# Optimization experiments

Hardware: AMD Instinct MI355X
Metric: run time of the kernel (lower is better)

## Reference

```python
import jax, jax.numpy as jnp
import numpy as np

N = 200000   # nodes
E = 6400000  # edges (avg degree 32)
T = 6        # member feature dim
M = 10       # fingerprint dim
L = 4        # R + 1 layers
GIN = 14     # group_level_input
GLO = 10     # group_level_output


def setup_inputs() -> dict:
    key = jax.random.key(0)
    ks = jax.random.split(key, 10)
    return {
        "x_member": jax.random.normal(ks[0], (N, T), dtype=jnp.float32),
        "x_group": jax.random.normal(ks[1], (1, GIN), dtype=jnp.float32),
        "src": jax.random.randint(ks[2], (E,), 0, N, dtype=jnp.int32),
        "dst": jax.random.randint(ks[3], (E,), 0, N, dtype=jnp.int32),
        "H": jax.random.normal(ks[4], (L, T, M), dtype=jnp.float32),
        "W": jax.random.normal(ks[5], (L,), dtype=jnp.float32),
        "gW": jax.random.normal(ks[6], (GLO, GIN), dtype=jnp.float32) * 0.1,
        "gb": jax.random.normal(ks[7], (GLO,), dtype=jnp.float32),
        "mW": jax.random.normal(ks[8], (3, M + GLO), dtype=jnp.float32) * 0.1,
        "mb": jax.random.normal(ks[9], (3,), dtype=jnp.float32),
    }


def reference(x_member, x_group, src, dst, H, W, gW, gb, mW, mb):
    n = x_member.shape[0]
    # message passing: neighbor feature sum per destination node  [N, T]
    neigh = jax.ops.segment_sum(x_member[src], dst, num_segments=n)
    v1 = x_member + neigh  # r[a] + sum of neighbor r's; r is layer-invariant
    # all R+1 layers at once: [L, N, M]
    v2 = jax.nn.sigmoid(jnp.einsum("nt,ltm->lnm", v1, H))
    fl = jax.nn.softmax(v2 * W[:, None, None], axis=-1)
    # f starts at zeros and accumulates softmax over every node and layer -> [1, M]
    f = jnp.sum(fl, axis=(0, 1))[None, :]
    # group-level perceptron
    g = jax.nn.sigmoid(x_group @ gW.T + gb)  # [1, GLO]
    merged = jnp.concatenate([f, g], axis=1)  # [1, M+GLO]
    return jax.nn.softmax(merged @ mW.T + mb, axis=-1)  # [1, 3]
```

## Files before the change

### kernel.cpp

```cpp
#include <hip/hip_runtime.h>
#include <hip/hip_fp16.h>
#include <math.h>

#define TDIM 6
#define MDIM 10
#define LDIM 4
#define GIND 14
#define GLOD 10

#define BINSHIFT 8
#define BINSZ 256
#define MAXBINS 1024

#define SC2_BLOCKS 1024
#define SC2_THREADS 512
#define SC2_CHQ 800
#define SC2_CHUNKS 2
#define SC2_TQ 2
#define OVF_ENT 16384
#define META2 2048

#define SC_BLOCK 512
#define SC_EPT 32
#define SC_EPB (SC_BLOCK * SC_EPT)
#define AC_BLOCK 512
#define AC_CAP 8704
#define AC_EPT 17

#define SRT_HALF 4352
#define AH_EPT 9
#define PB_NODE (BINSZ * TDIM)

__global__ void zero32_k(unsigned* __restrict__ p, int n) {
    int i = blockIdx.x * blockDim.x + threadIdx.x;
    if (i < n) p[i] = 0u;
}

__device__ __forceinline__ void add_row4(uint4 r, float& s0, float& s1, float& s2,
                                         float& s3, float& s4, float& s5) {
    float2 a0 = __half22float2(*(__half2*)&r.x);
    float2 a1 = __half22float2(*(__half2*)&r.y);
    float2 a2 = __half22float2(*(__half2*)&r.z);
    s0 += a0.x; s1 += a0.y; s2 += a1.x; s3 += a1.y; s4 += a2.x; s5 += a2.y;
}


__global__ __launch_bounds__(SC2_THREADS) void scat2_k(
        const float* __restrict__ xm, int N, uint4* __restrict__ xh,
        const int* __restrict__ src, const int* __restrict__ dst, int E, int NQ, int QPB,
        unsigned* __restrict__ gcount, unsigned* __restrict__ ebuf, int C, int nbins,
        uint2* __restrict__ ovf, unsigned* __restrict__ ocur) {
    __shared__ unsigned lcount[MAXBINS];
    __shared__ unsigned lbase[MAXBINS];
    __shared__ unsigned lcur[MAXBINS];
    __shared__ unsigned cstart[MAXBINS];
    __shared__ unsigned wsum[8];
    __shared__ unsigned spk[SC2_CHQ * 4];
    __shared__ unsigned short sbin[SC2_CHQ * 4];
    int tid = threadIdx.x;
    for (int i = tid; i < MAXBINS; i += SC2_THREADS) { lcount[i] = 0u; lcur[i] = 0u; }

    int gid = blockIdx.x * SC2_THREADS + tid;
    int gstride = gridDim.x * SC2_THREADS;
    for (int n = gid; n < N; n += gstride) {
        const float2* r = (const float2*)(xm + (size_t)n * TDIM);
        float2 a = r[0], b = r[1], c = r[2];
        __half2 h0 = __floats2half2_rn(a.x, a.y);
        __half2 h1 = __floats2half2_rn(b.x, b.y);
        __half2 h2 = __floats2half2_rn(c.x, c.y);
        uint4 o;
        o.x = *(unsigned*)&h0; o.y = *(unsigned*)&h1; o.z = *(unsigned*)&h2; o.w = 0u;
        xh[n] = o;
    }
    if (blockIdx.x == 0) {
        for (int e = NQ * 4 + tid; e < E; e += SC2_THREADS) {
            unsigned oc = atomicAdd(ocur, 1u);
            if (oc < OVF_ENT) ovf[oc] = make_uint2((unsigned)src[e], (unsigned)dst[e]);
        }
    }
    __syncthreads();

    int qb = blockIdx.x * QPB;
    int qend = qb + QPB; if (qend > NQ) qend = NQ;
    const int4* s4p = (const int4*)src;
    const int4* d4p = (const int4*)dst;

    for (int q = qb + tid; q < qend; q += SC2_THREADS) {
        int4 dv = d4p[q];
        atomicAdd(&lcount[((unsigned)dv.x) >> BINSHIFT], 1u);
        atomicAdd(&lcount[((unsigned)dv.y) >> BINSHIFT], 1u);
        atomicAdd(&lcount[((unsigned)dv.z) >> BINSHIFT], 1u);
        atomicAdd(&lcount[((unsigned)dv.w) >> BINSHIFT], 1u);
    }
    __syncthreads();
    for (int i = tid; i < nbins; i += SC2_THREADS) {
        unsigned c = lcount[i];
        if (c) lbase[i] = atomicAdd(&gcount[i], c);
    }
    __syncthreads();

    for (int ch = 0; ch < SC2_CHUNKS; ch++) {
        int cb = qb + ch * SC2_CHQ;
        if (cb >= qend) break;
        int ce = cb + SC2_CHQ; if (ce > qend) ce = qend;
        for (int i = tid; i < MAXBINS; i += SC2_THREADS) lcount[i] = 0u;
        __syncthreads();

        unsigned pk[SC2_TQ * 4];
        unsigned wr[SC2_TQ * 4];
#pragma unroll
        for (int i = 0; i < SC2_TQ; i++) {
            int q = cb + tid + i * SC2_THREADS;
            if (q < ce) {
                int4 sv = s4p[q];
                int4 dv = d4p[q];
                {
                    unsigned du = (unsigned)dv.x, b = du >> BINSHIFT;
                    pk[i*4+0] = ((du & (BINSZ-1)) << 18) | (unsigned)sv.x;
                    wr[i*4+0] = (b << 18) | atomicAdd(&lcount[b], 1u);
                }
                {
                    unsigned du = (unsigned)dv.y, b = du >> BINSHIFT;
                    pk[i*4+1] = ((du & (BINSZ-1)) << 18) | (unsigned)sv.y;
                    wr[i*4+1] = (b << 18) | atomicAdd(&lcount[b], 1u);
                }
                {
                    unsigned du = (unsigned)dv.z, b = du >> BINSHIFT;
                    pk[i*4+2] = ((du & (BINSZ-1)) << 18) | (unsigned)sv.z;
                    wr[i*4+2] = (b << 18) | atomicAdd(&lcount[b], 1u);
                }
                {
                    unsigned du = (unsigned)dv.w, b = du >> BINSHIFT;
                    pk[i*4+3] = ((du & (BINSZ-1)) << 18) | (unsigned)sv.w;
                    wr[i*4+3] = (b << 18) | atomicAdd(&lcount[b], 1u);
                }
            } else {
                pk[i*4+0] = 0xFFFFFFFFu; pk[i*4+1] = 0xFFFFFFFFu;
                pk[i*4+2] = 0xFFFFFFFFu; pk[i*4+3] = 0xFFFFFFFFu;
            }
        }
        __syncthreads();

        unsigned a0 = lcount[2*tid], a1 = lcount[2*tid+1];
        {
            unsigned s = a0 + a1;
            int lane = tid & 63;
#pragma unroll
            for (int off = 1; off < 64; off <<= 1) {
                unsigned t = (unsigned)__shfl_up((int)s, off, 64);
                if (lane >= off) s += t;
            }
            if (lane == 63) wsum[tid >> 6] = s;
            __syncthreads();
            unsigned add = 0; int w = tid >> 6;
#pragma unroll
            for (int ww = 0; ww < 7; ww++) if (ww < w) add += wsum[ww];
            unsigned excl = s + add - (a0 + a1);
            cstart[2*tid] = excl;
            cstart[2*tid+1] = excl + a0;
        }
        __syncthreads();

#pragma unroll
        for (int k = 0; k < SC2_TQ * 4; k++) {
            unsigned p = pk[k];
            if (p != 0xFFFFFFFFu) {
                unsigned b = wr[k] >> 18;
                unsigned r = wr[k] & 0x3FFFFu;
                unsigned li = cstart[b] + r;
                spk[li] = p;
                sbin[li] = (unsigned short)b;
            }
        }
        __syncthreads();

        unsigned T = cstart[MAXBINS-1] + lcount[MAXBINS-1];
        for (unsigned j = tid; j < T; j += SC2_THREADS) {
            unsigned p = spk[j];
            unsigned b = (unsigned)sbin[j];
            unsigned pos = lbase[b] + lcur[b] + (j - cstart[b]);
            if (pos < (unsigned)C) {
                ebuf[b * (unsigned)C + pos] = p;
            } else {
                unsigned oc = atomicAdd(ocur, 1u);
                if (oc < OVF_ENT) {
                    ovf[oc] = make_uint2(p & 0x3FFFFu,
                                         (b << BINSHIFT) | (p >> 18));
                }
            }
        }
        lcur[2*tid]   += a0;
        lcur[2*tid+1] += a1;
        __syncthreads();
    }
}

__global__ __launch_bounds__(512) void accum_a_k(
        const uint4* __restrict__ xh,
        const unsigned* __restrict__ ebuf, const unsigned* __restrict__ gcount, int C,
        const unsigned* __restrict__ ocur, const uint2* __restrict__ ovf,
        float* __restrict__ pbuf, int nbins) {
    __shared__ unsigned srt[SRT_HALF];
    __shared__ unsigned cnt[BINSZ];
    __shared__ unsigned cstart[BINSZ];
    __shared__ unsigned wsum[4];
    __shared__ unsigned ovl[256];
    __shared__ unsigned ovn;
    float (*part)[BINSZ][TDIM] = (float(*)[BINSZ][TDIM])srt;
    int tid = threadIdx.x;
    int bh = blockIdx.x;
    int bin = bh >> 1;
    unsigned half = (unsigned)(bh & 1);
    if (tid < BINSZ) cnt[tid] = 0u;
    if (tid == 0) ovn = 0u;
    __syncthreads();

    unsigned gc = gcount[bin];
    unsigned m = gc < (unsigned)C ? gc : (unsigned)C;
    unsigned lo = half ? (m >> 1) : 0u;
    unsigned hi = half ? m : (m >> 1);
    unsigned e0 = (unsigned)bin * (unsigned)C;

    unsigned ed_[AH_EPT];
    unsigned rk_[AH_EPT];
#pragma unroll
    for (int k = 0; k < AH_EPT; k++) {
        ed_[k] = 0xFFFFFFFFu;
        unsigned i = lo + (unsigned)tid + (unsigned)k * 512u;
        if (i < hi) {
            unsigned v = __builtin_nontemporal_load(ebuf + e0 + i);
            ed_[k] = v;
            rk_[k] = atomicAdd(&cnt[v >> 18], 1u);
        }
    }
    if (half == 0u) {
        unsigned novf = *ocur;
        if (novf > OVF_ENT) novf = OVF_ENT;
        for (unsigned i = tid; i < novf; i += 512u) {
            uint2 e = ovf[i];
            if ((e.y >> BINSHIFT) == (unsigned)bin) {
                unsigned u = atomicAdd(&ovn, 1u);
                if (u < 256u) ovl[u] = ((e.y & (BINSZ-1)) << 18) | e.x;
            }
        }
    }
    __syncthreads();

    {
        unsigned v = (tid < BINSZ) ? cnt[tid] : 0u;
        int lane = tid & 63;
#pragma unroll
        for (int off = 1; off < 64; off <<= 1) {
            unsigned t = (unsigned)__shfl_up((int)v, off, 64);
            if (lane >= off) v += t;
        }
        if (tid < BINSZ && lane == 63) wsum[tid >> 6] = v;
        __syncthreads();
        if (tid < BINSZ) {
            unsigned add = 0;
            int w = tid >> 6;
#pragma unroll
            for (int ww = 0; ww < 3; ww++) if (ww < w) add += wsum[ww];
            cstart[tid] = v + add - cnt[tid];
        }
        __syncthreads();
    }

#pragma unroll
    for (int k = 0; k < AH_EPT; k++) {
        unsigned v = ed_[k];
        if (v != 0xFFFFFFFFu) srt[cstart[v >> 18] + rk_[k]] = v & 0x3FFFFu;
    }
    __syncthreads();

    int node = tid & (BINSZ - 1);
    int role = tid >> 8;
    float s0 = 0.f, s1 = 0.f, s2 = 0.f, s3 = 0.f, s4 = 0.f, s5 = 0.f;
    {
        unsigned c = cnt[node];
        unsigned b0 = cstart[node];
        unsigned h2 = c >> 1;
        unsigned j  = role ? h2 : 0u;
        unsigned je = role ? c : h2;
        for (; j + 8 <= je; j += 8) {
            unsigned i0 = srt[b0 + j],     i1 = srt[b0 + j + 1];
            unsigned i2 = srt[b0 + j + 2], i3 = srt[b0 + j + 3];
            unsigned i4 = srt[b0 + j + 4], i5 = srt[b0 + j + 5];
            unsigned i6 = srt[b0 + j + 6], i7 = srt[b0 + j + 7];
            uint4 r0 = xh[i0], r1 = xh[i1], r2 = xh[i2], r3 = xh[i3];
            uint4 r4 = xh[i4], r5 = xh[i5], r6 = xh[i6], r7 = xh[i7];
            add_row4(r0, s0, s1, s2, s3, s4, s5);
            add_row4(r1, s0, s1, s2, s3, s4, s5);
            add_row4(r2, s0, s1, s2, s3, s4, s5);
            add_row4(r3, s0, s1, s2, s3, s4, s5);
            add_row4(r4, s0, s1, s2, s3, s4, s5);
            add_row4(r5, s0, s1, s2, s3, s4, s5);
            add_row4(r6, s0, s1, s2, s3, s4, s5);
            add_row4(r7, s0, s1, s2, s3, s4, s5);
        }
        for (; j + 2 <= je; j += 2) {
            unsigned ia = srt[b0 + j], ib = srt[b0 + j + 1];
            uint4 ra = xh[ia], rb = xh[ib];
            add_row4(ra, s0, s1, s2, s3, s4, s5);
            add_row4(rb, s0, s1, s2, s3, s4, s5);
        }
        if (j < je) {
            uint4 ra = xh[srt[b0 + j]];
            add_row4(ra, s0, s1, s2, s3, s4, s5);
        }
        if (role == 0) {
            unsigned no = ovn < 256u ? ovn : 256u;
            for (unsigned q = 0; q < no; q++) {
                unsigned o = ovl[q];
                if ((int)(o >> 18) == node) {
                    uint4 rr = xh[o & 0x3FFFFu];
                    add_row4(rr, s0, s1, s2, s3, s4, s5);
                }
            }
        }
    }
    __syncthreads();
    part[role][node][0] = s0; part[role][node][1] = s1; part[role][node][2] = s2;
    part[role][node][3] = s3; part[role][node][4] = s4; part[role][node][5] = s5;
    __syncthreads();

    float* pb = pbuf + (size_t)bh * PB_NODE;
    for (int j = tid; j < PB_NODE; j += 512) {
        int nd = j / TDIM, d = j - nd * TDIM;
        pb[j] = part[0][nd][d] + part[1][nd][d];
    }
}

__global__ __launch_bounds__(256) void accum_b_k(
        const float* __restrict__ xm, const float* __restrict__ pbuf,
        const float* __restrict__ H, const float* __restrict__ W,
        float* __restrict__ facc, int N) {
    __shared__ float sH[LDIM * TDIM * MDIM];
    __shared__ float sW[LDIM];
    __shared__ float sred[4][MDIM];
    int tid = threadIdx.x;
    for (int i = tid; i < LDIM * TDIM * MDIM; i += 256) sH[i] = H[i];
    if (tid < LDIM) sW[tid] = W[tid];
    __syncthreads();

    int n = blockIdx.x * 256 + tid;
    float fs[MDIM];
#pragma unroll
    for (int mm = 0; mm < MDIM; mm++) fs[mm] = 0.f;

    if (n < N) {
        int bin = n >> BINSHIFT;
        int node = n & (BINSZ - 1);
        const float* p0 = pbuf + (size_t)(bin * 2 + 0) * PB_NODE + node * TDIM;
        const float* p1 = pbuf + (size_t)(bin * 2 + 1) * PB_NODE + node * TDIM;
        const float2* xr = (const float2*)(xm + (size_t)n * TDIM);
        float2 x0 = xr[0], x1 = xr[1], x2 = xr[2];
        float v[TDIM];
        v[0] = x0.x + p0[0] + p1[0];
        v[1] = x0.y + p0[1] + p1[1];
        v[2] = x1.x + p0[2] + p1[2];
        v[3] = x1.y + p0[3] + p1[3];
        v[4] = x2.x + p0[4] + p1[4];
        v[5] = x2.y + p0[5] + p1[5];

#pragma unroll
        for (int l = 0; l < LDIM; l++) {
            float z[MDIM];
#pragma unroll
            for (int mm = 0; mm < MDIM; mm++) {
                float a2 = 0.f;
#pragma unroll
                for (int t = 0; t < TDIM; t++) a2 += v[t] * sH[(l * TDIM + t) * MDIM + mm];
                z[mm] = a2;
            }
            float wl = sW[l];
            float mx = -1e30f;
#pragma unroll
            for (int mm = 0; mm < MDIM; mm++) {
                float sg = wl / (1.f + __expf(-z[mm]));
                z[mm] = sg;
                mx = fmaxf(mx, sg);
            }
            float se = 0.f;
#pragma unroll
            for (int mm = 0; mm < MDIM; mm++) {
                float e = __expf(z[mm] - mx);
                z[mm] = e;
                se += e;
            }
            float inv = 1.f / se;
#pragma unroll
            for (int mm = 0; mm < MDIM; mm++) fs[mm] += z[mm] * inv;
        }
    }

#pragma unroll
    for (int mm = 0; mm < MDIM; mm++) {
        float v = fs[mm];
#pragma unroll
        for (int off = 32; off > 0; off >>= 1) v += __shfl_down(v, off, 64);
        fs[mm] = v;
    }
    int wave = tid >> 6, lane = tid & 63;
    if (lane == 0) {
#pragma unroll
        for (int mm = 0; mm < MDIM; mm++) sred[wave][mm] = fs[mm];
    }
    __syncthreads();
    if (tid < MDIM) {
        float s = 0.f;
#pragma unroll
        for (int w = 0; w < 4; w++) s += sred[w][tid];
        atomicAdd(facc + tid, s);
    }
}

__global__ __launch_bounds__(AC_BLOCK) void accum2_k(
        const float* __restrict__ xm, const uint4* __restrict__ xh,
        const unsigned* __restrict__ ebuf, const unsigned* __restrict__ gcount, int C,
        const unsigned* __restrict__ ocur, const uint2* __restrict__ ovf,
        const float* __restrict__ H, const float* __restrict__ W,
        float* __restrict__ facc, int N) {
    __shared__ unsigned srt[AC_CAP];
    __shared__ unsigned cnt[BINSZ];
    __shared__ unsigned cstart[BINSZ];
    __shared__ unsigned wsum[8];
    __shared__ unsigned ovl[256];
    __shared__ unsigned ovn;
    __shared__ float sH[LDIM * TDIM * MDIM];
    __shared__ float sW[LDIM];
    __shared__ float sred[AC_BLOCK / 64][MDIM];
    float (*part)[BINSZ][TDIM] = (float(*)[BINSZ][TDIM])srt;
    int tid = threadIdx.x;
    int bin = blockIdx.x;
    for (int i = tid; i < LDIM * TDIM * MDIM; i += AC_BLOCK) sH[i] = H[i];
    if (tid < LDIM) sW[tid] = W[tid];
    if (tid < BINSZ) cnt[tid] = 0u;
    if (tid == 0) ovn = 0u;
    __syncthreads();

    unsigned gc = gcount[bin];
    unsigned m = gc < (unsigned)C ? gc : (unsigned)C;
    unsigned e0 = (unsigned)bin * (unsigned)C;
    int nbase = bin << BINSHIFT;

    unsigned ed_[AC_EPT];
    unsigned rk_[AC_EPT];
#pragma unroll
    for (int k = 0; k < AC_EPT; k++) {
        unsigned i = (unsigned)tid + (unsigned)k * AC_BLOCK;
        if (i < m) {
            unsigned v = __builtin_nontemporal_load(ebuf + e0 + i);
            ed_[k] = v;
            rk_[k] = atomicAdd(&cnt[v >> 18], 1u);
        }
    }
    {
        unsigned novf = *ocur;
        if (novf > OVF_ENT) novf = OVF_ENT;
        for (unsigned i = tid; i < novf; i += AC_BLOCK) {
            uint2 e = ovf[i];
            if ((e.y >> BINSHIFT) == (unsigned)bin) {
                unsigned u = atomicAdd(&ovn, 1u);
                if (u < 256u) ovl[u] = ((e.y & (BINSZ-1)) << 18) | e.x;
            }
        }
    }
    __syncthreads();

    {
        unsigned v = (tid < BINSZ) ? cnt[tid] : 0u;
        int lane = tid & 63;
#pragma unroll
        for (int off = 1; off < 64; off <<= 1) {
            unsigned t = (unsigned)__shfl_up((int)v, off, 64);
            if (lane >= off) v += t;
        }
        if (tid < BINSZ && lane == 63) wsum[tid >> 6] = v;
        __syncthreads();
        if (tid < BINSZ) {
            unsigned add = 0;
            int w = tid >> 6;
#pragma unroll
            for (int ww = 0; ww < 3; ww++) if (ww < w) add += wsum[ww];
            cstart[tid] = v + add - cnt[tid];
        }
        __syncthreads();
    }

#pragma unroll
    for (int k = 0; k < AC_EPT; k++) {
        unsigned i = (unsigned)tid + (unsigned)k * AC_BLOCK;
        if (i < m) {
            unsigned v = ed_[k];
            srt[cstart[v >> 18] + rk_[k]] = v & 0x3FFFFu;
        }
    }
    __syncthreads();

    int node = tid & (BINSZ - 1);
    int role = tid >> 8;
    int n = nbase + node;
    float s0 = 0.f, s1 = 0.f, s2 = 0.f, s3 = 0.f, s4 = 0.f, s5 = 0.f;
    if (n < N) {
        unsigned c = cnt[node];
        unsigned b0 = cstart[node];
        unsigned h = c >> 1;
        unsigned j  = role ? h : 0u;
        unsigned je = role ? c : h;
        for (; j + 8 <= je; j += 8) {
            unsigned i0 = srt[b0 + j],     i1 = srt[b0 + j + 1];
            unsigned i2 = srt[b0 + j + 2], i3 = srt[b0 + j + 3];
            unsigned i4 = srt[b0 + j + 4], i5 = srt[b0 + j + 5];
            unsigned i6 = srt[b0 + j + 6], i7 = srt[b0 + j + 7];
            uint4 r0 = xh[i0], r1 = xh[i1], r2 = xh[i2], r3 = xh[i3];
            uint4 r4 = xh[i4], r5 = xh[i5], r6 = xh[i6], r7 = xh[i7];
            add_row4(r0, s0, s1, s2, s3, s4, s5);
            add_row4(r1, s0, s1, s2, s3, s4, s5);
            add_row4(r2, s0, s1, s2, s3, s4, s5);
            add_row4(r3, s0, s1, s2, s3, s4, s5);
            add_row4(r4, s0, s1, s2, s3, s4, s5);
            add_row4(r5, s0, s1, s2, s3, s4, s5);
            add_row4(r6, s0, s1, s2, s3, s4, s5);
            add_row4(r7, s0, s1, s2, s3, s4, s5);
        }
        for (; j + 2 <= je; j += 2) {
            unsigned ia = srt[b0 + j], ib = srt[b0 + j + 1];
            uint4 ra = xh[ia], rb = xh[ib];
            add_row4(ra, s0, s1, s2, s3, s4, s5);
            add_row4(rb, s0, s1, s2, s3, s4, s5);
        }
        if (j < je) {
            uint4 ra = xh[srt[b0 + j]];
            add_row4(ra, s0, s1, s2, s3, s4, s5);
        }
        if (role == 0) {
            unsigned no = ovn < 256u ? ovn : 256u;
            for (unsigned q = 0; q < no; q++) {
                unsigned o = ovl[q];
                if ((int)(o >> 18) == node) {
                    uint4 rr = xh[o & 0x3FFFFu];
                    add_row4(rr, s0, s1, s2, s3, s4, s5);
                }
            }
        }
    }
    __syncthreads();
    part[role][node][0] = s0; part[role][node][1] = s1; part[role][node][2] = s2;
    part[role][node][3] = s3; part[role][node][4] = s4; part[role][node][5] = s5;
    __syncthreads();

    float fs[MDIM];
#pragma unroll
    for (int mm = 0; mm < MDIM; mm++) fs[mm] = 0.f;

    if (n < N) {
        float v[TDIM];
        const float2* xr = (const float2*)(xm + (size_t)n * TDIM);
        float2 x0 = xr[0], x1 = xr[1], x2 = xr[2];
        v[0] = x0.x + part[0][node][0] + part[1][node][0];
        v[1] = x0.y + part[0][node][1] + part[1][node][1];
        v[2] = x1.x + part[0][node][2] + part[1][node][2];
        v[3] = x1.y + part[0][node][3] + part[1][node][3];
        v[4] = x2.x + part[0][node][4] + part[1][node][4];
        v[5] = x2.y + part[0][node][5] + part[1][node][5];

        int lb = role << 1;
#pragma unroll
        for (int li = 0; li < 2; li++) {
            int l = lb + li;
            float z[MDIM];
#pragma unroll
            for (int mm = 0; mm < MDIM; mm++) {
                float a2 = 0.f;
#pragma unroll
                for (int t = 0; t < TDIM; t++) a2 += v[t] * sH[(l * TDIM + t) * MDIM + mm];
                z[mm] = a2;
            }
            float wl = sW[l];
            float mx = -1e30f;
#pragma unroll
            for (int mm = 0; mm < MDIM; mm++) {
                float sg = wl / (1.f + __expf(-z[mm]));
                z[mm] = sg;
                mx = fmaxf(mx, sg);
            }
            float se = 0.f;
#pragma unroll
            for (int mm = 0; mm < MDIM; mm++) {
                float e = __expf(z[mm] - mx);
                z[mm] = e;
                se += e;
            }
            float inv = 1.f / se;
#pragma unroll
            for (int mm = 0; mm < MDIM; mm++) fs[mm] += z[mm] * inv;
        }
    }

#pragma unroll
    for (int mm = 0; mm < MDIM; mm++) {
        float v = fs[mm];
#pragma unroll
        for (int off = 32; off > 0; off >>= 1) v += __shfl_down(v, off, 64);
        fs[mm] = v;
    }
    int wave = tid >> 6, lane = tid & 63;
    if (lane == 0) {
#pragma unroll
        for (int mm = 0; mm < MDIM; mm++) sred[wave][mm] = fs[mm];
    }
    __syncthreads();
    if (tid < MDIM) {
        float s = 0.f;
#pragma unroll
        for (int w = 0; w < AC_BLOCK / 64; w++) s += sred[w][tid];
        atomicAdd(facc + tid, s);
    }
}


__global__ __launch_bounds__(256) void prep_k(const float* __restrict__ xm, int N,
                                              uint4* __restrict__ xh,
                                              const int* __restrict__ dst, int E,
                                              unsigned* __restrict__ hist, int nbins) {
    __shared__ unsigned lh[MAXBINS];
    for (int i = threadIdx.x; i < MAXBINS; i += blockDim.x) lh[i] = 0u;
    __syncthreads();
    int gid = blockIdx.x * blockDim.x + threadIdx.x;
    int gstride = gridDim.x * blockDim.x;
    for (int n = gid; n < N; n += gstride) {
        const float2* r = (const float2*)(xm + (size_t)n * TDIM);
        float2 a = r[0], b = r[1], c = r[2];
        __half2 h0 = __floats2half2_rn(a.x, a.y);
        __half2 h1 = __floats2half2_rn(b.x, b.y);
        __half2 h2 = __floats2half2_rn(c.x, c.y);
        uint4 o;
        o.x = *(unsigned*)&h0; o.y = *(unsigned*)&h1; o.z = *(unsigned*)&h2; o.w = 0u;
        xh[n] = o;
    }
    int e4 = E >> 2;
    const int4* d4p = (const int4*)dst;
    for (int i = gid; i < e4; i += gstride) {
        int4 d = d4p[i];
        atomicAdd(&lh[((unsigned)d.x) >> BINSHIFT], 1u);
        atomicAdd(&lh[((unsigned)d.y) >> BINSHIFT], 1u);
        atomicAdd(&lh[((unsigned)d.z) >> BINSHIFT], 1u);
        atomicAdd(&lh[((unsigned)d.w) >> BINSHIFT], 1u);
    }
    for (int e = (e4 << 2) + gid; e < E; e += gstride)
        atomicAdd(&lh[((unsigned)dst[e]) >> BINSHIFT], 1u);
    __syncthreads();
    for (int i = threadIdx.x; i < nbins; i += blockDim.x)
        if (lh[i]) atomicAdd(&hist[i], lh[i]);
}

__global__ __launch_bounds__(MAXBINS) void scan_k(const unsigned* __restrict__ hist,
                                                  unsigned* __restrict__ offsets,
                                                  unsigned* __restrict__ gfill, int nbins) {
    __shared__ unsigned buf[2][MAXBINS];
    int t = threadIdx.x;
    buf[0][t] = (t < nbins) ? hist[t] : 0u;
    __syncthreads();
    int cur = 0;
    for (int off = 1; off < MAXBINS; off <<= 1) {
        unsigned v = buf[cur][t];
        if (t >= off) v += buf[cur][t - off];
        buf[cur ^ 1][t] = v;
        __syncthreads();
        cur ^= 1;
    }
    if (t < nbins) {
        unsigned ex = t ? buf[cur][t - 1] : 0u;
        offsets[t] = ex;
        gfill[t] = ex;
    }
    if (t == 0) offsets[nbins] = buf[cur][nbins - 1];
}

__global__ __launch_bounds__(SC_BLOCK) void scatter_k(const int* __restrict__ src,
                                                      const int* __restrict__ dst, int E,
                                                      unsigned* __restrict__ gfill,
                                                      unsigned* __restrict__ ebuf, int nbins) {
    __shared__ unsigned lcount[MAXBINS];
    __shared__ unsigned lbase[MAXBINS];
    for (int i = threadIdx.x; i < MAXBINS; i += SC_BLOCK) lcount[i] = 0u;
    __syncthreads();
    int base = blockIdx.x * SC_EPB + threadIdx.x * SC_EPT;
    int s[SC_EPT], d[SC_EPT];
    unsigned rk[SC_EPT];
#pragma unroll
    for (int q = 0; q < SC_EPT / 4; q++) {
        int e = base + q * 4;
        if (e + 3 < E) {
            int4 s4 = *(const int4*)(src + e);
            int4 d4 = *(const int4*)(dst + e);
            s[q*4+0] = s4.x; s[q*4+1] = s4.y; s[q*4+2] = s4.z; s[q*4+3] = s4.w;
            d[q*4+0] = d4.x; d[q*4+1] = d4.y; d[q*4+2] = d4.z; d[q*4+3] = d4.w;
        } else {
#pragma unroll
            for (int k = 0; k < 4; k++) {
                int ee = e + k;
                s[q*4+k] = (ee < E) ? src[ee] : -1;
                d[q*4+k] = (ee < E) ? dst[ee] : 0;
            }
        }
    }
#pragma unroll
    for (int k = 0; k < SC_EPT; k++)
        if (s[k] >= 0) rk[k] = atomicAdd(&lcount[((unsigned)d[k]) >> BINSHIFT], 1u);
    __syncthreads();
    for (int i = threadIdx.x; i < nbins; i += SC_BLOCK) {
        unsigned c = lcount[i];
        if (c) lbase[i] = atomicAdd(&gfill[i], c);
    }
    __syncthreads();
#pragma unroll
    for (int k = 0; k < SC_EPT; k++) {
        if (s[k] >= 0) {
            unsigned du = (unsigned)d[k];
            unsigned b = du >> BINSHIFT;
            unsigned pack = ((du & (BINSZ - 1)) << 18) | (unsigned)s[k];
            ebuf[lbase[b] + rk[k]] = pack;
        }
    }
}

__global__ __launch_bounds__(AC_BLOCK) void accum_node_k(
        const float* __restrict__ xm, const uint4* __restrict__ xh,
        const unsigned* __restrict__ ebuf, const unsigned* __restrict__ offsets,
        const float* __restrict__ H, const float* __restrict__ W,
        float* __restrict__ facc, int N) {
    __shared__ unsigned srt[AC_CAP];
    __shared__ unsigned cnt[BINSZ];
    __shared__ unsigned tmp[BINSZ];
    __shared__ unsigned cstart[BINSZ];
    __shared__ float sH[LDIM * TDIM * MDIM];
    __shared__ float sW[LDIM];
    __shared__ float sred[AC_BLOCK / 64][MDIM];
    int tid = threadIdx.x;
    int bin = blockIdx.x;
    for (int i = tid; i < LDIM * TDIM * MDIM; i += AC_BLOCK) sH[i] = H[i];
    if (tid < LDIM) sW[tid] = W[tid];
    if (tid < BINSZ) cnt[tid] = 0u;
    __syncthreads();

    unsigned e0 = offsets[bin], e1 = offsets[bin + 1];
    unsigned total = e1 - e0;
    unsigned m = total < AC_CAP ? total : AC_CAP;
    int nbase = bin << BINSHIFT;

    unsigned ed_[AC_EPT];
    unsigned rk_[AC_EPT];
#pragma unroll
    for (int k = 0; k < AC_EPT; k++) {
        unsigned idx = e0 + (unsigned)tid + (unsigned)k * AC_BLOCK;
        if (idx < e0 + m) {
            unsigned v = ebuf[idx];
            ed_[k] = v;
            rk_[k] = atomicAdd(&cnt[v >> 18], 1u);
        }
    }
    __syncthreads();

    if (tid < BINSZ) tmp[tid] = cnt[tid];
    __syncthreads();
    for (int off = 1; off < BINSZ; off <<= 1) {
        unsigned v = 0;
        if (tid < BINSZ) { v = tmp[tid]; if (tid >= off) v += tmp[tid - off]; }
        __syncthreads();
        if (tid < BINSZ) tmp[tid] = v;
        __syncthreads();
    }
    if (tid < BINSZ) cstart[tid] = tmp[tid] - cnt[tid];
    __syncthreads();

#pragma unroll
    for (int k = 0; k < AC_EPT; k++) {
        unsigned idx = e0 + (unsigned)tid + (unsigned)k * AC_BLOCK;
        if (idx < e0 + m) {
            unsigned v = ed_[k];
            srt[cstart[v >> 18] + rk_[k]] = v & 0x3FFFFu;
        }
    }
    __syncthreads();

    float fs[MDIM];
#pragma unroll
    for (int mm = 0; mm < MDIM; mm++) fs[mm] = 0.f;

    int n = nbase + tid;
    if (tid < BINSZ && n < N) {
        float s0 = 0.f, s1 = 0.f, s2 = 0.f, s3 = 0.f, s4 = 0.f, s5 = 0.f;
        unsigned c = cnt[tid];
        unsigned b0 = cstart[tid];
        unsigned j = 0;
        for (; j + 2 <= c; j += 2) {
            unsigned sa = srt[b0 + j], sb = srt[b0 + j + 1];
            uint4 ra = xh[sa];
            uint4 rb = xh[sb];
            add_row4(ra, s0, s1, s2, s3, s4, s5);
            add_row4(rb, s0, s1, s2, s3, s4, s5);
        }
        if (j < c) {
            uint4 ra = xh[srt[b0 + j]];
            add_row4(ra, s0, s1, s2, s3, s4, s5);
        }
        for (unsigned idx = e0 + m; idx < e1; idx++) {
            unsigned v = ebuf[idx];
            if ((int)(v >> 18) == tid) {
                uint4 ra = xh[v & 0x3FFFFu];
                add_row4(ra, s0, s1, s2, s3, s4, s5);
            }
        }

        float v[TDIM];
        const float2* xr = (const float2*)(xm + (size_t)n * TDIM);
        float2 x0 = xr[0], x1 = xr[1], x2 = xr[2];
        v[0] = x0.x + s0; v[1] = x0.y + s1;
        v[2] = x1.x + s2; v[3] = x1.y + s3;
        v[4] = x2.x + s4; v[5] = x2.y + s5;

#pragma unroll
        for (int l = 0; l < LDIM; l++) {
            float z[MDIM];
#pragma unroll
            for (int mm = 0; mm < MDIM; mm++) {
                float a2 = 0.f;
#pragma unroll
                for (int t = 0; t < TDIM; t++) a2 += v[t] * sH[(l * TDIM + t) * MDIM + mm];
                z[mm] = a2;
            }
            float wl = sW[l];
            float mx = -1e30f;
#pragma unroll
            for (int mm = 0; mm < MDIM; mm++) {
                float sg = wl / (1.f + __expf(-z[mm]));
                z[mm] = sg;
                mx = fmaxf(mx, sg);
            }
            float se = 0.f;
#pragma unroll
            for (int mm = 0; mm < MDIM; mm++) {
                float e = __expf(z[mm] - mx);
                z[mm] = e;
                se += e;
            }
            float inv = 1.f / se;
#pragma unroll
            for (int mm = 0; mm < MDIM; mm++) fs[mm] += z[mm] * inv;
        }
    }

#pragma unroll
    for (int mm = 0; mm < MDIM; mm++) {
        float v = fs[mm];
#pragma unroll
        for (int off = 32; off > 0; off >>= 1) v += __shfl_down(v, off, 64);
        fs[mm] = v;
    }
    int wave = tid >> 6, lane = tid & 63;
    if (lane == 0) {
#pragma unroll
        for (int mm = 0; mm < MDIM; mm++) sred[wave][mm] = fs[mm];
    }
    __syncthreads();
    if (tid < MDIM) {
        float s = 0.f;
#pragma unroll
        for (int w = 0; w < AC_BLOCK / 64; w++) s += sred[w][tid];
        atomicAdd(facc + tid, s);
    }
}

__global__ void finalize_k(const float* __restrict__ facc,
                           const float* __restrict__ xg,
                           const float* __restrict__ gW,
                           const float* __restrict__ gb,
                           const float* __restrict__ mW,
                           const float* __restrict__ mb,
                           float* __restrict__ out) {
    if (threadIdx.x == 0 && blockIdx.x == 0) {
        float merged[MDIM + GLOD];
#pragma unroll
        for (int m = 0; m < MDIM; m++) merged[m] = facc[m];
        for (int j = 0; j < GLOD; j++) {
            float a = gb[j];
            for (int i = 0; i < GIND; i++) a += xg[i] * gW[j * GIND + i];
            merged[MDIM + j] = 1.f / (1.f + __expf(-a));
        }
        float lg[3];
        float mx = -1e30f;
        for (int k = 0; k < 3; k++) {
            float a = mb[k];
            for (int j = 0; j < MDIM + GLOD; j++) a += merged[j] * mW[k * (MDIM + GLOD) + j];
            lg[k] = a;
            mx = fmaxf(mx, a);
        }
        float se = 0.f;
        for (int k = 0; k < 3; k++) { lg[k] = __expf(lg[k] - mx); se += lg[k]; }
        float inv = 1.f / se;
        for (int k = 0; k < 3; k++) out[k] = lg[k] * inv;
    }
}

__global__ void fb_zero_k(float* __restrict__ ws, int n) {
    int i = blockIdx.x * blockDim.x + threadIdx.x;
    if (i < n) ws[i] = 0.f;
}

__global__ void fb_edge_scatter_k(const float* __restrict__ xm,
                                  const int* __restrict__ src,
                                  const int* __restrict__ dst,
                                  float* __restrict__ neigh, int E) {
    int e = blockIdx.x * blockDim.x + threadIdx.x;
    if (e >= E) return;
    int s = src[e], d = dst[e];
    const float2* r = (const float2*)(xm + (size_t)s * TDIM);
    float2 a = r[0], b = r[1], c = r[2];
    float* o = neigh + (size_t)d * TDIM;
    atomicAdd(o + 0, a.x); atomicAdd(o + 1, a.y);
    atomicAdd(o + 2, b.x); atomicAdd(o + 3, b.y);
    atomicAdd(o + 4, c.x); atomicAdd(o + 5, c.y);
}

__global__ __launch_bounds__(256) void fb_node_k(
        const float* __restrict__ xm, const float* __restrict__ neigh,
        const float* __restrict__ H, const float* __restrict__ W,
        float* __restrict__ facc, int N) {
    __shared__ float sH[LDIM * TDIM * MDIM];
    __shared__ float sW[LDIM];
    __shared__ float sred[4][MDIM];
    int tid = threadIdx.x;
    for (int i = tid; i < LDIM * TDIM * MDIM; i += blockDim.x) sH[i] = H[i];
    if (tid < LDIM) sW[tid] = W[tid];
    __syncthreads();
    float fs[MDIM];
#pragma unroll
    for (int m = 0; m < MDIM; m++) fs[m] = 0.f;
    for (int n = blockIdx.x * blockDim.x + tid; n < N; n += gridDim.x * blockDim.x) {
        float v[TDIM];
        const float2* xr = (const float2*)(xm + (size_t)n * TDIM);
        const float2* nr = (const float2*)(neigh + (size_t)n * TDIM);
#pragma unroll
        for (int t2 = 0; t2 < 3; t2++) {
            float2 a = xr[t2], b = nr[t2];
            v[2 * t2 + 0] = a.x + b.x;
            v[2 * t2 + 1] = a.y + b.y;
        }
#pragma unroll
        for (int l = 0; l < LDIM; l++) {
            float z[MDIM];
#pragma unroll
            for (int m = 0; m < MDIM; m++) {
                float a2 = 0.f;
#pragma unroll
                for (int t = 0; t < TDIM; t++) a2 += v[t] * sH[(l * TDIM + t) * MDIM + m];
                z[m] = a2;
            }
            float wl = sW[l], mx = -1e30f;
#pragma unroll
            for (int m = 0; m < MDIM; m++) { float sg = wl / (1.f + __expf(-z[m])); z[m] = sg; mx = fmaxf(mx, sg); }
            float se = 0.f;
#pragma unroll
            for (int m = 0; m < MDIM; m++) { float e = __expf(z[m] - mx); z[m] = e; se += e; }
            float inv = 1.f / se;
#pragma unroll
            for (int m = 0; m < MDIM; m++) fs[m] += z[m] * inv;
        }
    }
#pragma unroll
    for (int m = 0; m < MDIM; m++) {
        float v = fs[m];
#pragma unroll
        for (int off = 32; off > 0; off >>= 1) v += __shfl_down(v, off, 64);
        fs[m] = v;
    }
    int wave = tid >> 6, lane = tid & 63;
    if (lane == 0) {
#pragma unroll
        for (int m = 0; m < MDIM; m++) sred[wave][m] = fs[m];
    }
    __syncthreads();
    if (tid < MDIM) {
        float s = sred[0][tid] + sred[1][tid] + sred[2][tid] + sred[3][tid];
        atomicAdd(facc + tid, s);
    }
}

extern "C" void kernel_launch(void* const* d_in, const int* in_sizes, int n_in,
                              void* d_out, int out_size, void* d_ws, size_t ws_size,
                              hipStream_t stream) {
    const float* xm  = (const float*)d_in[0];
    const float* xg  = (const float*)d_in[1];
    const int*   src = (const int*)d_in[2];
    const int*   dst = (const int*)d_in[3];
    const float* H   = (const float*)d_in[4];
    const float* W   = (const float*)d_in[5];
    const float* gW  = (const float*)d_in[6];
    const float* gb  = (const float*)d_in[7];
    const float* mW  = (const float*)d_in[8];
    const float* mb  = (const float*)d_in[9];
    float* out = (float*)d_out;

    int N = in_sizes[0] / TDIM;
    int E = in_sizes[2];
    int nbins = (N + BINSZ - 1) >> BINSHIFT;
    size_t ws_words = ws_size / 4;
    size_t xh_words = (size_t)N * 4;
    size_t pbuf_words = (size_t)nbins * 2 * PB_NODE;

    double mu = (double)E / nbins;
    long Cmin = (long)(mu + 4.0 * sqrt(mu) + 32.0);
    int NQ = E >> 2;
    int QPB = (NQ + SC2_BLOCKS - 1) / SC2_BLOCKS;
    bool qpb_ok = QPB <= SC2_CHUNKS * SC2_CHQ;

    long fixed_s = (long)(xh_words + META2 + (size_t)OVF_ENT * 2 + pbuf_words);
    long avail_s = (long)ws_words - fixed_s;
    long Cs = avail_s > 0 ? (avail_s / nbins) & ~3L : 0;
    if (Cs > AC_CAP) Cs = AC_CAP;
    bool ok1s = (Cs >= Cmin) && nbins <= MAXBINS && N <= (1 << 18) && qpb_ok;

    long fixed = (long)(xh_words + META2 + (size_t)OVF_ENT * 2);
    long avail = (long)ws_words - fixed;
    long C = avail > 0 ? (avail / nbins) & ~3L : 0;
    if (C > AC_CAP) C = AC_CAP;
    bool ok1 = (C >= Cmin) && nbins <= MAXBINS && N <= (1 << 18) && qpb_ok;

    size_t meta_words2 = MAXBINS + (MAXBINS + 1) + MAXBINS + 16;
    size_t need2 = (xh_words + (size_t)E + meta_words2) * 4;
    bool ok2 = ws_size >= need2 && nbins <= MAXBINS && N <= (1 << 18);

    if (ok1s) {
        uint4*    xh     = (uint4*)d_ws;
        unsigned* ebuf   = (unsigned*)d_ws + xh_words;
        unsigned* gcount = ebuf + (size_t)nbins * Cs;
        unsigned* ocur   = gcount + MAXBINS;
        float*    facc   = (float*)(ocur + 16);
        uint2*    ovf    = (uint2*)(gcount + META2);
        float*    pbuf   = (float*)(gcount + META2 + (size_t)OVF_ENT * 2);

        zero32_k<<<(META2 + 255) / 256, 256, 0, stream>>>(gcount, META2);
        scat2_k<<<SC2_BLOCKS, SC2_THREADS, 0, stream>>>(xm, N, xh, src, dst, E, NQ, QPB,
                                                        gcount, ebuf, (int)Cs, nbins, ovf, ocur);
        accum_a_k<<<nbins * 2, 512, 0, stream>>>(xh, ebuf, gcount, (int)Cs, ocur, ovf,
                                                 pbuf, nbins);
        accum_b_k<<<(N + 255) / 256, 256, 0, stream>>>(xm, pbuf, H, W, facc, N);
        finalize_k<<<1, 64, 0, stream>>>(facc, xg, gW, gb, mW, mb, out);
    } else if (ok1) {
        uint4*    xh     = (uint4*)d_ws;
        unsigned* ebuf   = (unsigned*)d_ws + xh_words;
        unsigned* gcount = ebuf + (size_t)nbins * C;
        unsigned* ocur   = gcount + MAXBINS;
        float*    facc   = (float*)(ocur + 16);
        uint2*    ovf    = (uint2*)(gcount + META2);

        zero32_k<<<(META2 + 255) / 256, 256, 0, stream>>>(gcount, META2);
        scat2_k<<<SC2_BLOCKS, SC2_THREADS, 0, stream>>>(xm, N, xh, src, dst, E, NQ, QPB,
                                                        gcount, ebuf, (int)C, nbins, ovf, ocur);
        accum2_k<<<nbins, AC_BLOCK, 0, stream>>>(xm, xh, ebuf, gcount, (int)C, ocur, ovf,
                                                 H, W, facc, N);
        finalize_k<<<1, 64, 0, stream>>>(facc, xg, gW, gb, mW, mb, out);
    } else if (ok2) {
        uint4*    xh      = (uint4*)d_ws;
        unsigned* ebuf    = (unsigned*)d_ws + xh_words;
        unsigned* hist    = ebuf + (size_t)E;
        unsigned* offsets = hist + MAXBINS;
        unsigned* gfill   = offsets + MAXBINS + 1;
        float*    facc    = (float*)(gfill + MAXBINS);

        zero32_k<<<(int)((meta_words2 + 255) / 256), 256, 0, stream>>>(hist, (int)meta_words2);
        prep_k<<<1024, 256, 0, stream>>>(xm, N, xh, dst, E, hist, nbins);
        scan_k<<<1, MAXBINS, 0, stream>>>(hist, offsets, gfill, nbins);
        scatter_k<<<(E + SC_EPB - 1) / SC_EPB, SC_BLOCK, 0, stream>>>(src, dst, E, gfill, ebuf, nbins);
        accum_node_k<<<nbins, AC_BLOCK, 0, stream>>>(xm, xh, ebuf, offsets, H, W, facc, N);
        finalize_k<<<1, 64, 0, stream>>>(facc, xg, gW, gb, mW, mb, out);
    } else {
        float* neigh = (float*)d_ws;
        float* facc  = neigh + (size_t)N * TDIM;
        int zn = N * TDIM + 16;
        fb_zero_k<<<(zn + 255) / 256, 256, 0, stream>>>(neigh, zn);
        fb_edge_scatter_k<<<(E + 255) / 256, 256, 0, stream>>>(xm, src, dst, neigh, E);
        fb_node_k<<<256, 256, 0, stream>>>(xm, neigh, H, W, facc, N);
        finalize_k<<<1, 64, 0, stream>>>(facc, xg, gW, gb, mW, mb, out);
    }
}
```

Before: 127.7 us.

## Fuse edge binning count pass into a single register-held load with chunk snapshots

The scatter kernel no longer reads dst twice, once for a separate per-bin counting pass and again per chunk. Each thread now loads all its src/dst quads once into registers and assigns local ranks with shared atomics. It snapshots the per-bin counts at chunk boundaries so the later chunked shared-memory sort and global write can recover per-chunk offsets. Block count and chunk sizes are retuned to fit that layout. The aim is to remove one full pass of global dst traffic, at the cost of more registers per thread and extra barriers for the snapshots.

```diff
diff --git a/kernel.cpp b/kernel.cpp
--- a/kernel.cpp
+++ b/kernel.cpp
@@ -12,11 +12,11 @@
 #define BINSZ 256
 #define MAXBINS 1024
 
-#define SC2_BLOCKS 1024
+#define SC2_BLOCKS 768
 #define SC2_THREADS 512
-#define SC2_CHQ 800
-#define SC2_CHUNKS 2
-#define SC2_TQ 2
+#define SC2_KQ 5
+#define SC2_CHQ 1024
+#define SC2_NCH 3
 #define OVF_ENT 16384
 #define META2 2048
 
@@ -52,13 +52,13 @@
         uint2* __restrict__ ovf, unsigned* __restrict__ ocur) {
     __shared__ unsigned lcount[MAXBINS];
     __shared__ unsigned lbase[MAXBINS];
-    __shared__ unsigned lcur[MAXBINS];
+    __shared__ unsigned snap[SC2_NCH - 1][MAXBINS];
     __shared__ unsigned cstart[MAXBINS];
     __shared__ unsigned wsum[8];
     __shared__ unsigned spk[SC2_CHQ * 4];
     __shared__ unsigned short sbin[SC2_CHQ * 4];
     int tid = threadIdx.x;
-    for (int i = tid; i < MAXBINS; i += SC2_THREADS) { lcount[i] = 0u; lcur[i] = 0u; }
+    for (int i = tid; i < MAXBINS; i += SC2_THREADS) lcount[i] = 0u;
 
     int gid = blockIdx.x * SC2_THREADS + tid;
     int gstride = gridDim.x * SC2_THREADS;
@@ -85,63 +85,61 @@
     const int4* s4p = (const int4*)src;
     const int4* d4p = (const int4*)dst;
 
-    for (int q = qb + tid; q < qend; q += SC2_THREADS) {
-        int4 dv = d4p[q];
-        atomicAdd(&lcount[((unsigned)dv.x) >> BINSHIFT], 1u);
-        atomicAdd(&lcount[((unsigned)dv.y) >> BINSHIFT], 1u);
-        atomicAdd(&lcount[((unsigned)dv.z) >> BINSHIFT], 1u);
-        atomicAdd(&lcount[((unsigned)dv.w) >> BINSHIFT], 1u);
-    }
-    __syncthreads();
+    unsigned pk[SC2_KQ * 4];
+    unsigned wr[SC2_KQ * 4];
+
+#pragma unroll
+    for (int i = 0; i < SC2_KQ; i++) {
+        int q = qb + tid + i * SC2_THREADS;
+        if (q < qend) {
+            int4 sv = s4p[q];
+            int4 dv = d4p[q];
+            {
+                unsigned du = (unsigned)dv.x, b = du >> BINSHIFT;
+                pk[i*4+0] = ((du & (BINSZ-1)) << 18) | (unsigned)sv.x;
+                wr[i*4+0] = (b << 18) | atomicAdd(&lcount[b], 1u);
+            }
+            {
+                unsigned du = (unsigned)dv.y, b = du >> BINSHIFT;
+                pk[i*4+1] = ((du & (BINSZ-1)) << 18) | (unsigned)sv.y;
+                wr[i*4+1] = (b << 18) | atomicAdd(&lcount[b], 1u);
+            }
+            {
+                unsigned du = (unsigned)dv.z, b = du >> BINSHIFT;
+                pk[i*4+2] = ((du & (BINSZ-1)) << 18) | (unsigned)sv.z;
+                wr[i*4+2] = (b << 18) | atomicAdd(&lcount[b], 1u);
+            }
+            {
+                unsigned du = (unsigned)dv.w, b = du >> BINSHIFT;
+                pk[i*4+3] = ((du & (BINSZ-1)) << 18) | (unsigned)sv.w;
+                wr[i*4+3] = (b << 18) | atomicAdd(&lcount[b], 1u);
+            }
+        } else {
+            pk[i*4+0] = 0xFFFFFFFFu; pk[i*4+1] = 0xFFFFFFFFu;
+            pk[i*4+2] = 0xFFFFFFFFu; pk[i*4+3] = 0xFFFFFFFFu;
+        }
+        if (i == 1 || i == 3) {
+            __syncthreads();
+            for (int b2 = tid; b2 < MAXBINS; b2 += SC2_THREADS)
+                snap[i >> 1][b2] = lcount[b2];
+            __syncthreads();
+        }
+    }
+    __syncthreads();
+
     for (int i = tid; i < nbins; i += SC2_THREADS) {
         unsigned c = lcount[i];
         if (c) lbase[i] = atomicAdd(&gcount[i], c);
     }
     __syncthreads();
 
-    for (int ch = 0; ch < SC2_CHUNKS; ch++) {
-        int cb = qb + ch * SC2_CHQ;
-        if (cb >= qend) break;
-        int ce = cb + SC2_CHQ; if (ce > qend) ce = qend;
-        for (int i = tid; i < MAXBINS; i += SC2_THREADS) lcount[i] = 0u;
-        __syncthreads();
-
-        unsigned pk[SC2_TQ * 4];
-        unsigned wr[SC2_TQ * 4];
-#pragma unroll
-        for (int i = 0; i < SC2_TQ; i++) {
-            int q = cb + tid + i * SC2_THREADS;
-            if (q < ce) {
-                int4 sv = s4p[q];
-                int4 dv = d4p[q];
-                {
-                    unsigned du = (unsigned)dv.x, b = du >> BINSHIFT;
-                    pk[i*4+0] = ((du & (BINSZ-1)) << 18) | (unsigned)sv.x;
-                    wr[i*4+0] = (b << 18) | atomicAdd(&lcount[b], 1u);
-                }
-                {
-                    unsigned du = (unsigned)dv.y, b = du >> BINSHIFT;
-                    pk[i*4+1] = ((du & (BINSZ-1)) << 18) | (unsigned)sv.y;
-                    wr[i*4+1] = (b << 18) | atomicAdd(&lcount[b], 1u);
-                }
-                {
-                    unsigned du = (unsigned)dv.z, b = du >> BINSHIFT;
-                    pk[i*4+2] = ((du & (BINSZ-1)) << 18) | (unsigned)sv.z;
-                    wr[i*4+2] = (b << 18) | atomicAdd(&lcount[b], 1u);
-                }
-                {
-                    unsigned du = (unsigned)dv.w, b = du >> BINSHIFT;
-                    pk[i*4+3] = ((du & (BINSZ-1)) << 18) | (unsigned)sv.w;
-                    wr[i*4+3] = (b << 18) | atomicAdd(&lcount[b], 1u);
-                }
-            } else {
-                pk[i*4+0] = 0xFFFFFFFFu; pk[i*4+1] = 0xFFFFFFFFu;
-                pk[i*4+2] = 0xFFFFFFFFu; pk[i*4+3] = 0xFFFFFFFFu;
-            }
-        }
-        __syncthreads();
-
-        unsigned a0 = lcount[2*tid], a1 = lcount[2*tid+1];
+#pragma unroll
+    for (int ch = 0; ch < SC2_NCH; ch++) {
+        unsigned p0 = (ch == 0) ? 0u : snap[ch-1][2*tid];
+        unsigned p1 = (ch == 0) ? 0u : snap[ch-1][2*tid+1];
+        unsigned e0v = (ch == SC2_NCH-1) ? lcount[2*tid]   : snap[ch][2*tid];
+        unsigned e1v = (ch == SC2_NCH-1) ? lcount[2*tid+1] : snap[ch][2*tid+1];
+        unsigned a0 = e0v - p0, a1 = e1v - p1;
         {
             unsigned s = a0 + a1;
             int lane = tid & 63;
@@ -162,23 +160,30 @@
         __syncthreads();
 
 #pragma unroll
-        for (int k = 0; k < SC2_TQ * 4; k++) {
-            unsigned p = pk[k];
-            if (p != 0xFFFFFFFFu) {
-                unsigned b = wr[k] >> 18;
-                unsigned r = wr[k] & 0x3FFFFu;
-                unsigned li = cstart[b] + r;
-                spk[li] = p;
-                sbin[li] = (unsigned short)b;
+        for (int i = ch * 2; i < ((ch * 2 + 2 < SC2_KQ) ? ch * 2 + 2 : SC2_KQ); i++) {
+#pragma unroll
+            for (int kk = 0; kk < 4; kk++) {
+                unsigned p = pk[i*4 + kk];
+                if (p != 0xFFFFFFFFu) {
+                    unsigned b = wr[i*4 + kk] >> 18;
+                    unsigned prevb = (ch == 0) ? 0u : snap[ch-1][b];
+                    unsigned local = (wr[i*4 + kk] & 0x3FFFFu) - prevb;
+                    unsigned li = cstart[b] + local;
+                    spk[li] = p;
+                    sbin[li] = (unsigned short)b;
+                }
             }
         }
         __syncthreads();
 
-        unsigned T = cstart[MAXBINS-1] + lcount[MAXBINS-1];
+        unsigned lastp = (ch == 0) ? 0u : snap[ch-1][MAXBINS-1];
+        unsigned laste = (ch == SC2_NCH-1) ? lcount[MAXBINS-1] : snap[ch][MAXBINS-1];
+        unsigned T = cstart[MAXBINS-1] + (laste - lastp);
         for (unsigned j = tid; j < T; j += SC2_THREADS) {
             unsigned p = spk[j];
             unsigned b = (unsigned)sbin[j];
-            unsigned pos = lbase[b] + lcur[b] + (j - cstart[b]);
+            unsigned prevb = (ch == 0) ? 0u : snap[ch-1][b];
+            unsigned pos = lbase[b] + prevb + (j - cstart[b]);
             if (pos < (unsigned)C) {
                 ebuf[b * (unsigned)C + pos] = p;
             } else {
@@ -189,8 +194,6 @@
                 }
             }
         }
-        lcur[2*tid]   += a0;
-        lcur[2*tid+1] += a1;
         __syncthreads();
     }
 }
@@ -1014,7 +1017,7 @@
     long Cmin = (long)(mu + 4.0 * sqrt(mu) + 32.0);
     int NQ = E >> 2;
     int QPB = (NQ + SC2_BLOCKS - 1) / SC2_BLOCKS;
-    bool qpb_ok = QPB <= SC2_CHUNKS * SC2_CHQ;
+    bool qpb_ok = QPB <= SC2_KQ * SC2_THREADS;
 
     long fixed_s = (long)(xh_words + META2 + (size_t)OVF_ENT * 2 + pbuf_words);
     long avail_s = (long)ws_words - fixed_s;
```

Result: faster. 116.0 us (-9.2%).
